# Kernel tuning notes

Hardware: AMD Instinct MI355X
Metric: run time of the kernel (lower is better)

Reference implementation:

```python
import jax, jax.numpy as jnp
import numpy as np

B, P, S, D, H, DFF, VOC = 8, 16, 512, 512, 8, 2048, 10000
DEPTH = D // H
SIGMA = 0.1
T = 256
LN_EPS = 1e-6


def setup_inputs() -> dict:
    key = jax.random.key(0)
    ks = jax.random.split(key, 40)
    n = lambda i, sh, sc=1.0: jax.random.normal(ks[i], sh, jnp.float32) * sc
    inp = {
        "r": n(0, (B, P, D)),
        "x": jax.random.randint(ks[1], (B, 1), 0, VOC),
        "K": n(2, (B, P, S, D)),
        "Vs": n(3, (B, P, S, D)),
        "w": jax.random.uniform(ks[4], (B, P, 1), jnp.float32),
        "I": jax.random.randint(ks[5], (B, P, S), 0, P),
        "t": T,
        "eps_q": n(6, (B, P, 1, D)),
        "eps_k": n(7, (B, P, 1, D)),
        "eps_v": n(8, (B, P, 1, D)),
        "eps_z": n(9, (B, P, 1, D)),
        "gumbel": -jnp.log(-jnp.log(jax.random.uniform(ks[10], (B, P, P), jnp.float32, 1e-8, 1.0))),
        "Wq": n(11, (D, D), 0.02), "bq": jnp.zeros((D,), jnp.float32),
        "Wk": n(12, (D, D), 0.02), "bk": jnp.zeros((D,), jnp.float32),
        "Wv": n(13, (D, D), 0.02), "bv": jnp.zeros((D,), jnp.float32),
        "Wo": n(14, (D, D), 0.02), "bo": jnp.zeros((D,), jnp.float32),
        "ln1_g": jnp.ones((D,), jnp.float32), "ln1_b": jnp.zeros((D,), jnp.float32),
        "ln3_g": jnp.ones((D,), jnp.float32), "ln3_b": jnp.zeros((D,), jnp.float32),
        "W1": n(15, (D, DFF), 0.02), "b1": jnp.zeros((DFF,), jnp.float32),
        "W2": n(16, (DFF, D), 0.02), "b2": jnp.zeros((D,), jnp.float32),
        "Wout": n(17, (D, VOC), 0.02), "bout": jnp.zeros((VOC,), jnp.float32),
    }
    return inp


def _layernorm(x, g, b):
    mu = jnp.mean(x, axis=-1, keepdims=True)
    var = jnp.mean((x - mu) ** 2, axis=-1, keepdims=True)
    return (x - mu) / jnp.sqrt(var + LN_EPS) * g + b


def _split_heads(x):  # (B,P,L,D) -> (B,P,H,L,depth)
    b, p, l, _ = x.shape
    return x.reshape(b, p, l, H, DEPTH).transpose(0, 1, 3, 2, 4)


def _resample(params, i_t, t):  # reorder particle axis on prefix [:t+1]
    pref = jnp.take_along_axis(params[:, :, :t + 1], i_t[:, :, None, None], axis=1)
    return jnp.concatenate([pref, params[:, :, t + 1:]], axis=2)


def reference(r, x, K, Vs, w, I, t, eps_q, eps_k, eps_v, eps_z, gumbel,
              Wq, bq, Wk, bk, Wv, bv, Wo, bo, ln1_g, ln1_b, ln3_g, ln3_b,
              W1, b1, W2, b2, Wout, bout):
    x = x.astype(jnp.int32)
    I = I.astype(jnp.int32)
    r4 = r[:, :, None, :]                                   # (B,P,1,D)
    # --- mha_smc: noisy projections + K/V buffer update at t ---
    q = r4 @ Wq + bq + SIGMA * eps_q
    k = r4 @ Wk + bk + SIGMA * eps_k
    v = r4 @ Wv + bv + SIGMA * eps_v
    K = K.at[:, :, t, :].set(k[:, :, 0, :])
    Vs = Vs.at[:, :, t, :].set(v[:, :, 0, :])
    qh = _split_heads(q)                                    # (B,P,H,1,depth)
    Kh = _split_heads(K)                                    # (B,P,H,S,depth)
    Vh = _split_heads(Vs)
    scores = jnp.einsum('bphqd,bphsd->bphqs', qh, Kh) / jnp.sqrt(jnp.float32(DEPTH))
    mask = (jnp.arange(S) <= t)[None, None, None, None, :]
    scores = jnp.where(mask, scores, jnp.float32(-1e9))
    attn = jax.nn.softmax(scores, axis=-1)                  # (B,P,H,1,S)
    zh = jnp.einsum('bphqs,bphsd->bphqd', attn, Vh)
    z = zh.transpose(0, 1, 3, 2, 4).reshape(B, P, 1, D) @ Wo + bo
    z = z + SIGMA * eps_z                                   # reparametrized output noise
    attn_weights = jnp.mean(attn, axis=2)                   # (B,P,1,S)
    # --- residual + FFN (dropout disabled: training=False) ---
    out1 = _layernorm(z + r4, ln1_g, ln1_b)
    ffn = jnp.maximum(out1 @ W1 + b1, 0.0) @ W2 + b2
    r_ = _layernorm(ffn + out1, ln3_g, ln3_b)
    predictions = r_ @ Wout + bout                          # (B,P,1,VOC)
    # --- classification importance weights ---
    probs = jax.nn.softmax(predictions, axis=-1)
    idx = jnp.broadcast_to(x.reshape(B, 1, 1, 1), (B, P, 1, 1))
    w_sq = jnp.take_along_axis(probs, idx, axis=-1)[:, :, 0, 0]  # (B,P)
    w_sq = jax.lax.stop_gradient(w_sq)
    pred2 = predictions[:, :, 0, :]                         # (B,P,VOC)
    w_for_pred = w_sq[:, :, None]
    good_avg_pred = jnp.mean(pred2, axis=1, keepdims=True)  # (B,1,VOC)
    avg_pred_after_softmax = jnp.mean(jax.nn.softmax(pred2, axis=-1), axis=1, keepdims=True)
    argmax_w = jnp.argmax(w_for_pred, axis=1)               # (B,1)
    max_prediction = jnp.take_along_axis(pred2, argmax_w[:, :, None], axis=1)  # (B,1,VOC)
    # --- sample_and_keep_indices: Gumbel-max categorical over particles ---
    logits = jnp.log(w_sq + 1e-10)                          # (B,P)
    i_t = jnp.argmax(logits[:, None, :] + gumbel, axis=-1).astype(jnp.int32)  # (B,P)
    I_pref = jnp.take_along_axis(I[:, :, :t], i_t[:, :, None], axis=1)
    I_new = jnp.concatenate([I_pref, i_t[:, :, None], I[:, :, t + 1:]], axis=2)
    # --- resampling (faithful to original: V resampled from already-resampled K) ---
    K = _resample(K, i_t, t)
    Vs = _resample(K, i_t, t)
    z = jnp.take_along_axis(z, I_new[:, :, t][:, :, None, None], axis=1)
    w_new = w_sq[:, :, None]
    return (r4, z, avg_pred_after_softmax, good_avg_pred, max_prediction,
            eps_z, attn_weights, K, Vs, w_new, I_new)
```

## Files before the change

### kernel.cpp

```cpp
#include <hip/hip_runtime.h>

#define NDFF 2048
#define NVOC 10000
#define SIGMA 0.1f

typedef float f32x4 __attribute__((ext_vector_type(4)));

#define O0 0
#define O1 65536
#define O2 131072
#define O3 211072
#define O4 291072
#define O5 371072
#define O6 436608
#define O7 502144
#define O8 34056576
#define O9 67611008
#define O10 67611136

#define WQ    0
#define WK    65536
#define WV    131072
#define WZH   196608
#define WZ    262144
#define WO1   327680
#define WH1   393216
#define WPRED 720896
#define WMAX  2000896
#define WSUM  2001024
#define WWSQ  2001152
#define WIT   2001280
#define WF2P  2001536
#define WSC   2263680

__device__ __forceinline__ void copy_sgt(const float* __restrict__ Kin,
                                         float* __restrict__ out, int t,
                                         int q, int bid, int nblk, int tid, int nthr)
{
    const f32x4* K4 = (const f32x4*)Kin;
    f32x4* oK = (f32x4*)(out + O7);
    f32x4* oV = (f32x4*)(out + O8);
    int cnt = 511 - t;
    long totalc = (long)128 * cnt * 128;
    long q0 = (totalc * q) >> 2, q1 = (totalc * (q + 1)) >> 2;
    for (long j = q0 + (long)bid * nthr + tid; j < q1; j += (long)nblk * nthr) {
        int lane = (int)(j & 127);
        long row = j >> 7;
        int bp = (int)(row / cnt);
        int s = t + 1 + (int)(row - (long)bp * cnt);
        long i = ((long)(bp * 512 + s) << 7) + lane;
        f32x4 v = __builtin_nontemporal_load(&K4[i]);
        __builtin_nontemporal_store(v, &oK[i]);
        __builtin_nontemporal_store(v, &oV[i]);
    }
}

__global__ __launch_bounds__(512)
void k_qkv(const float* __restrict__ r,
           const float* __restrict__ Wq, const float* __restrict__ bq, const float* __restrict__ eq, float* __restrict__ oq,
           const float* __restrict__ Wk, const float* __restrict__ bk, const float* __restrict__ ek, float* __restrict__ ok,
           const float* __restrict__ Wv, const float* __restrict__ bv, const float* __restrict__ ev, float* __restrict__ ov)
{
    const float *W, *bias, *eps; float* out;
    if (blockIdx.z == 0)      { W = Wq; bias = bq; eps = eq; out = oq; }
    else if (blockIdx.z == 1) { W = Wk; bias = bk; eps = ek; out = ok; }
    else                      { W = Wv; bias = bv; eps = ev; out = ov; }
    int tid = threadIdx.x;
    int col = tid & 63, kq = tid >> 6;
    int colg = blockIdx.x * 64 + col;
    int row0 = blockIdx.y * 8;
    __shared__ float rs[8][512];
#pragma unroll
    for (int j = 0; j < 8; j++) rs[j][tid & 511] = r[(row0 + j) * 512 + tid];
    __syncthreads();
    float acc[8] = {0,0,0,0,0,0,0,0};
    const float* Wp = W + (kq * 64) * 512 + colg;
#pragma unroll 8
    for (int d = 0; d < 64; d++) {
        float wv = Wp[d * 512];
#pragma unroll
        for (int p = 0; p < 8; p++) acc[p] += rs[p][kq * 64 + d] * wv;
    }
    __syncthreads();
    float (*part)[8][64] = (float(*)[8][64])rs;
#pragma unroll
    for (int p = 0; p < 8; p++) part[kq][p][col] = acc[p];
    __syncthreads();
    {
        int p = tid >> 6, c = tid & 63;
        int cg = blockIdx.x * 64 + c;
        float v = 0.f;
#pragma unroll
        for (int k = 0; k < 8; k++) v += part[k][p][c];
        out[(row0 + p) * 512 + cg] = v + bias[cg] + SIGMA * eps[(row0 + p) * 512 + cg];
    }
}

__global__ __launch_bounds__(512)
void k_attn(const float* __restrict__ qws, const float* __restrict__ kws,
            const float* __restrict__ vws, const float* __restrict__ Kin,
            const float* __restrict__ Vin, const int* __restrict__ t_ptr,
            float* __restrict__ zh, float* __restrict__ scw)
{
    int t = *t_ptr;
    int bp = blockIdx.x, h = blockIdx.y;
    int tid = threadIdx.x;
    int wave = tid >> 6, lane = tid & 63;
    __shared__ float sc[512];
    __shared__ float red[8], red2[8];
    __shared__ float part[8][64];

    float4 qv = ((const float4*)(qws + bp * 512 + h * 64))[lane & 15];

    for (int sb = wave * 4; sb <= t; sb += 32) {
        int s = sb + (lane >> 4);
        bool valid = (s <= t);
        int ss = valid ? s : t;
        const float4* kr = (ss == t) ? (const float4*)(kws + bp * 512 + h * 64)
                                     : (const float4*)(Kin + (bp * 512 + ss) * 512 + h * 64);
        float4 kv = kr[lane & 15];
        float p = qv.x * kv.x + qv.y * kv.y + qv.z * kv.z + qv.w * kv.w;
#pragma unroll
        for (int m = 1; m < 16; m <<= 1) p += __shfl_xor(p, m, 64);
        if ((lane & 15) == 0 && valid) sc[s] = p * 0.125f;
    }
    __syncthreads();

    float lm = -3.0e38f;
    for (int s = tid; s <= t; s += 512) lm = fmaxf(lm, sc[s]);
#pragma unroll
    for (int o = 32; o; o >>= 1) lm = fmaxf(lm, __shfl_xor(lm, o, 64));
    if (lane == 0) red[wave] = lm;
    __syncthreads();
    float m = red[0];
#pragma unroll
    for (int i = 1; i < 8; i++) m = fmaxf(m, red[i]);
    float ls = 0.f;
    for (int s = tid; s <= t; s += 512) ls += __expf(sc[s] - m);
#pragma unroll
    for (int o = 32; o; o >>= 1) ls += __shfl_xor(ls, o, 64);
    if (lane == 0) red2[wave] = ls;
    __syncthreads();
    float tot = 0.f;
#pragma unroll
    for (int i = 0; i < 8; i++) tot += red2[i];
    float inv = 1.f / tot;
    for (int s = tid; s <= t; s += 512) {
        float a = __expf(sc[s] - m) * inv;
        sc[s] = a;
        scw[(bp * 8 + h) * 512 + s] = a;
    }
    __syncthreads();

    float acc = 0.f;
    const float* Vp = Vin + (bp * 512) * 512 + h * 64 + lane;
    int s = wave;
    for (; s + 24 < t; s += 32) {
        float v0 = __builtin_nontemporal_load(Vp + (size_t)(s     ) * 512);
        float v1 = __builtin_nontemporal_load(Vp + (size_t)(s +  8) * 512);
        float v2 = __builtin_nontemporal_load(Vp + (size_t)(s + 16) * 512);
        float v3 = __builtin_nontemporal_load(Vp + (size_t)(s + 24) * 512);
        acc += sc[s] * v0 + sc[s + 8] * v1 + sc[s + 16] * v2 + sc[s + 24] * v3;
    }
    for (; s < t; s += 8) acc += sc[s] * __builtin_nontemporal_load(Vp + (size_t)s * 512);
    if ((t & 7) == wave) acc += sc[t] * vws[bp * 512 + h * 64 + lane];
    part[wave][lane] = acc;
    __syncthreads();
    if (tid < 64) {
        float v = 0.f;
#pragma unroll
        for (int k = 0; k < 8; k++) v += part[k][tid];
        zh[bp * 512 + h * 64 + tid] = v;
    }
}

__global__ __launch_bounds__(512)
void k_zproj(const float* __restrict__ zh, const float* __restrict__ Wo,
             const float* __restrict__ bo, const float* __restrict__ epsz,
             const float* __restrict__ Kin, const int* __restrict__ t_ptr,
             float* __restrict__ outbuf, float* __restrict__ out)
{
    if (blockIdx.x >= 8) {
        int bid = (blockIdx.x - 8) * 16 + blockIdx.y;
        copy_sgt(Kin, outbuf, *t_ptr, 0, bid, 64, threadIdx.x, 512);
        return;
    }
    int tid = threadIdx.x;
    int col = tid & 63, kq = tid >> 6;
    int colg = blockIdx.x * 64 + col;
    int row0 = blockIdx.y * 8;
    __shared__ float rs[8][512];
#pragma unroll
    for (int j = 0; j < 8; j++) rs[j][tid] = zh[(row0 + j) * 512 + tid];
    __syncthreads();
    float acc[8] = {0,0,0,0,0,0,0,0};
    const float* Wp = Wo + (kq * 64) * 512 + colg;
#pragma unroll 8
    for (int d = 0; d < 64; d++) {
        float wv = Wp[d * 512];
#pragma unroll
        for (int p = 0; p < 8; p++) acc[p] += rs[p][kq * 64 + d] * wv;
    }
    __syncthreads();
    float (*part)[8][64] = (float(*)[8][64])rs;
#pragma unroll
    for (int p = 0; p < 8; p++) part[kq][p][col] = acc[p];
    __syncthreads();
    {
        int p = tid >> 6, c = tid & 63;
        int cg = blockIdx.x * 64 + c;
        float v = 0.f;
#pragma unroll
        for (int k = 0; k < 8; k++) v += part[k][p][c];
        out[(row0 + p) * 512 + cg] = v + bo[cg] + SIGMA * epsz[(row0 + p) * 512 + cg];
    }
}

__global__ __launch_bounds__(512)
void k_ffn1(const float* __restrict__ zp, const float* __restrict__ r,
            const float* __restrict__ g, const float* __restrict__ be,
            const float* __restrict__ W1, const float* __restrict__ b1,
            const float* __restrict__ Kin, const int* __restrict__ t_ptr,
            float* __restrict__ outbuf,
            float* __restrict__ o1, float* __restrict__ h1)
{
    if (blockIdx.x >= 32) {
        int bid = (blockIdx.x - 32) * 16 + blockIdx.y;
        copy_sgt(Kin, outbuf, *t_ptr, 1, bid, 64, threadIdx.x, 512);
        return;
    }
    int tid = threadIdx.x;
    int col = tid & 63, kq = tid >> 6;
    int colg = blockIdx.x * 64 + col;
    int row0 = blockIdx.y * 8;
    __shared__ float rs[8][512];
    __shared__ float sm[8], si[8];
    int wave = tid >> 6, lane = tid & 63;
#pragma unroll
    for (int j = 0; j < 8; j++) {
        int gi = (row0 + j) * 512 + tid;
        rs[j][tid] = zp[gi] + r[gi];
    }
    __syncthreads();
    {
        float s = 0.f;
        for (int c = lane; c < 512; c += 64) s += rs[wave][c];
#pragma unroll
        for (int o = 32; o; o >>= 1) s += __shfl_xor(s, o, 64);
        float mu = s * (1.f / 512.f);
        float v = 0.f;
        for (int c = lane; c < 512; c += 64) { float dx = rs[wave][c] - mu; v += dx * dx; }
#pragma unroll
        for (int o = 32; o; o >>= 1) v += __shfl_xor(v, o, 64);
        if (lane == 0) { sm[wave] = mu; si[wave] = rsqrtf(v * (1.f / 512.f) + 1e-6f); }
    }
    __syncthreads();
#pragma unroll
    for (int j = 0; j < 8; j++) {
        float val = (rs[j][tid] - sm[j]) * si[j] * g[tid] + be[tid];
        rs[j][tid] = val;
        if (blockIdx.x == 0) o1[(row0 + j) * 512 + tid] = val;
    }
    __syncthreads();
    float acc[8] = {0,0,0,0,0,0,0,0};
    const float* Wp = W1 + (kq * 64) * NDFF + colg;
#pragma unroll 8
    for (int d = 0; d < 64; d++) {
        float wv = Wp[d * NDFF];
#pragma unroll
        for (int p = 0; p < 8; p++) acc[p] += rs[p][kq * 64 + d] * wv;
    }
    __syncthreads();
    float (*part)[8][64] = (float(*)[8][64])rs;
#pragma unroll
    for (int p = 0; p < 8; p++) part[kq][p][col] = acc[p];
    __syncthreads();
    {
        int p = tid >> 6, c = tid & 63;
        int cg = blockIdx.x * 64 + c;
        float v = 0.f;
#pragma unroll
        for (int k = 0; k < 8; k++) v += part[k][p][c];
        h1[(row0 + p) * NDFF + cg] = fmaxf(v + b1[cg], 0.f);
    }
}

__global__ __launch_bounds__(512)
void k_ffn2p(const float* __restrict__ h1, const float* __restrict__ W2,
             const float* __restrict__ Kin, const int* __restrict__ t_ptr,
             float* __restrict__ outbuf, float* __restrict__ f2p)
{
    if (blockIdx.x >= 8) {
        int bid = blockIdx.y * 4 + blockIdx.z;
        copy_sgt(Kin, outbuf, *t_ptr, 2, bid, 64, threadIdx.x, 512);
        return;
    }
    int tid = threadIdx.x;
    int col = tid & 63, kq = tid >> 6;
    int colg = blockIdx.x * 64 + col;
    int row0 = blockIdx.y * 8;
    int ks = blockIdx.z;
    __shared__ float rs[8][512];
#pragma unroll
    for (int j = 0; j < 8; j++)
        rs[j][tid] = h1[(row0 + j) * NDFF + ks * 512 + tid];
    __syncthreads();
    float acc[8] = {0,0,0,0,0,0,0,0};
    const float* Wp = W2 + (ks * 512 + kq * 64) * 512 + colg;
#pragma unroll 8
    for (int d = 0; d < 64; d++) {
        float wv = Wp[d * 512];
#pragma unroll
        for (int p = 0; p < 8; p++) acc[p] += rs[p][kq * 64 + d] * wv;
    }
    __syncthreads();
    float (*part)[8][64] = (float(*)[8][64])rs;
#pragma unroll
    for (int p = 0; p < 8; p++) part[kq][p][col] = acc[p];
    __syncthreads();
    {
        int p = tid >> 6, c = tid & 63;
        int cg = blockIdx.x * 64 + c;
        float v = 0.f;
#pragma unroll
        for (int k = 0; k < 8; k++) v += part[k][p][c];
        f2p[ks * 65536 + (row0 + p) * 512 + cg] = v;
    }
}

__global__ __launch_bounds__(512)
void k_pred(const float* __restrict__ f2p, const float* __restrict__ b2,
            const float* __restrict__ o1, const float* __restrict__ g3,
            const float* __restrict__ b3, const float* __restrict__ Wout,
            const float* __restrict__ bout,
            const float* __restrict__ Kin, const int* __restrict__ t_ptr,
            float* __restrict__ outbuf, float* __restrict__ pred)
{
    if (blockIdx.x >= 40) {
        int bid = (blockIdx.x - 40) * 8 + blockIdx.y;
        copy_sgt(Kin, outbuf, *t_ptr, 3, bid, 64, threadIdx.x, 512);
        return;
    }
    int tid = threadIdx.x;
    int col = tid & 255, kh = tid >> 8;
    int colg = blockIdx.x * 256 + col;
    int colL = min(colg, NVOC - 1);
    int row0 = blockIdx.y * 16;
    __shared__ float rs[16][512];
    __shared__ float sm[16], si[16];
    int wave = tid >> 6, lane = tid & 63;
#pragma unroll
    for (int j = 0; j < 16; j++) {
        int gi = (row0 + j) * 512 + tid;
        rs[j][tid] = f2p[gi] + f2p[65536 + gi] + f2p[131072 + gi] + f2p[196608 + gi]
                   + b2[tid] + o1[gi];
    }
    __syncthreads();
    {
        int row = wave * 2 + (lane >> 5);
        int l = lane & 31;
        float s = 0.f;
        for (int c = l; c < 512; c += 32) s += rs[row][c];
#pragma unroll
        for (int o = 16; o; o >>= 1) s += __shfl_xor(s, o, 64);
        float mu = s * (1.f / 512.f);
        float v = 0.f;
        for (int c = l; c < 512; c += 32) { float dx = rs[row][c] - mu; v += dx * dx; }
#pragma unroll
        for (int o = 16; o; o >>= 1) v += __shfl_xor(v, o, 64);
        if (l == 0) { sm[row] = mu; si[row] = rsqrtf(v * (1.f / 512.f) + 1e-6f); }
    }
    __syncthreads();
#pragma unroll
    for (int j = 0; j < 16; j++)
        rs[j][tid] = (rs[j][tid] - sm[j]) * si[j] * g3[tid] + b3[tid];
    __syncthreads();
    float acc[16];
#pragma unroll
    for (int p = 0; p < 16; p++) acc[p] = 0.f;
    const float* Wp = Wout + (kh * 256) * NVOC + colL;
#pragma unroll 4
    for (int d = 0; d < 256; d++) {
        float wv = Wp[d * NVOC];
#pragma unroll
        for (int p = 0; p < 16; p++) acc[p] += rs[p][kh * 256 + d] * wv;
    }
    __syncthreads();
    float (*part)[256] = (float(*)[256])rs;
    if (kh == 1) {
#pragma unroll
        for (int p = 0; p < 16; p++) part[p][col] = acc[p];
    }
    __syncthreads();
    if (kh == 0 && colg < NVOC) {
        float bv = bout[colg];
#pragma unroll
        for (int p = 0; p < 16; p++)
            pred[(row0 + p) * NVOC + colg] = acc[p] + part[p][col] + bv;
    }
}

__global__ __launch_bounds__(512)
void k_soft(const float* __restrict__ pred, const int* __restrict__ x,
            const float* __restrict__ scw, const int* __restrict__ t_ptr,
            float* __restrict__ rowmax, float* __restrict__ rowsum,
            float* __restrict__ wsq, float* __restrict__ out)
{
    __shared__ float red[8];
    int row = blockIdx.x, tid = threadIdx.x;
    {
        int t = *t_ptr;
        float a = 0.f;
        if (tid <= t) {
#pragma unroll
            for (int hh = 0; hh < 8; hh++) a += scw[(row * 8 + hh) * 512 + tid];
            a *= 0.125f;
        }
        out[O6 + row * 512 + tid] = a;
    }
    const float* pr = pred + row * NVOC;
    float m = -3.0e38f;
    for (int v = tid; v < NVOC; v += 512) m = fmaxf(m, pr[v]);
#pragma unroll
    for (int o = 32; o; o >>= 1) m = fmaxf(m, __shfl_xor(m, o, 64));
    if ((tid & 63) == 0) red[tid >> 6] = m;
    __syncthreads();
#pragma unroll
    for (int i = 0; i < 8; i++) m = fmaxf(m, red[i]);
    __syncthreads();
    float s = 0.f;
    for (int v = tid; v < NVOC; v += 512) s += __expf(pr[v] - m);
#pragma unroll
    for (int o = 32; o; o >>= 1) s += __shfl_xor(s, o, 64);
    if ((tid & 63) == 0) red[tid >> 6] = s;
    __syncthreads();
    if (tid == 0) {
        float tot = 0.f;
#pragma unroll
        for (int i = 0; i < 8; i++) tot += red[i];
        rowmax[row] = m; rowsum[row] = tot;
        int b = row >> 4;
        float w = __expf(pr[x[b]] - m) / tot;
        wsq[row] = w;
        out[O9 + row] = w;
    }
}

__global__ __launch_bounds__(512)
void k_vocab(const float* __restrict__ pred, const float* __restrict__ rowmax,
             const float* __restrict__ rowsum, const float* __restrict__ wsq,
             const float* __restrict__ gumbel, int* __restrict__ it,
             float* __restrict__ out)
{
    int b = blockIdx.y;
    int tid = threadIdx.x;
    __shared__ int s_amw;
    if (tid == 0) {
        float bw = -3.0e38f; int bj = 0;
#pragma unroll
        for (int pp = 0; pp < 16; pp++) {
            float wv = wsq[b * 16 + pp];
            if (wv > bw) { bw = wv; bj = pp; }
        }
        s_amw = bj;
    }
    if (blockIdx.x == 0 && tid < 16) {
        float best = -3.0e38f; int bi = 0;
#pragma unroll
        for (int pp = 0; pp < 16; pp++) {
            float v = logf(wsq[b * 16 + pp] + 1e-10f) + gumbel[(b * 16 + tid) * 16 + pp];
            if (v > best) { best = v; bi = pp; }
        }
        it[b * 16 + tid] = bi;
    }
    __syncthreads();
    int v = blockIdx.x * 512 + tid;
    if (v >= NVOC) return;
    int amw = s_amw;
    float ga = 0.f, as = 0.f;
#pragma unroll
    for (int p = 0; p < 16; p++) {
        int rr = b * 16 + p;
        float pv = pred[rr * NVOC + v];
        ga += pv;
        as += __expf(pv - rowmax[rr]) * (1.f / rowsum[rr]);
    }
    out[O3 + b * NVOC + v] = ga * (1.f / 16.f);
    out[O2 + b * NVOC + v] = as * (1.f / 16.f);
    out[O4 + b * NVOC + v] = pred[(b * 16 + amw) * NVOC + v];
}

__global__ __launch_bounds__(256)
void k_resample(const float* __restrict__ Kin, const float* __restrict__ kws,
                const int* __restrict__ it, const int* __restrict__ t_ptr,
                const float* __restrict__ r, const float* __restrict__ epsz,
                const float* __restrict__ zws, const int* __restrict__ Iin,
                float* __restrict__ out)
{
    int t = *t_ptr;
    const f32x4* K4  = (const f32x4*)Kin;
    const f32x4* kw4 = (const f32x4*)kws;
    const f32x4* r4  = (const f32x4*)r;
    const f32x4* e4  = (const f32x4*)epsz;
    const f32x4* z4  = (const f32x4*)zws;
    f32x4* oK = (f32x4*)(out + O7);
    f32x4* oV = (f32x4*)(out + O8);
    int cnt = t + 1;
    long total = (long)128 * cnt * 128;
    long total2 = total + 16384;
    for (long j = (long)blockIdx.x * 256 + threadIdx.x; j < total2; j += (long)gridDim.x * 256) {
        if (j < total) {
            int lane = (int)(j & 127);
            long row = j >> 7;
            int bp = (int)(row / cnt);
            int s = (int)(row - (long)bp * cnt);
            int b = bp >> 4;
            int ip = it[bp];
            int ip2 = it[b * 16 + ip];
            f32x4 vK, vV;
            if (s == t) {
                vK = kw4[(b * 16 + ip) * 128 + lane];
                vV = kw4[(b * 16 + ip2) * 128 + lane];
            } else {
                vK = K4[((long)((b * 16 + ip) * 512 + s) << 7) + lane];
                vV = K4[((long)((b * 16 + ip2) * 512 + s) << 7) + lane];
            }
            long i = ((long)(bp * 512 + s) << 7) + lane;
            __builtin_nontemporal_store(vK, &oK[i]);
            __builtin_nontemporal_store(vV, &oV[i]);
        } else {
            int jj = (int)(j - total);
            int fidx = jj * 4;
            ((f32x4*)(out + O0))[jj] = r4[jj];
            ((f32x4*)(out + O5))[jj] = e4[jj];
            int row = fidx >> 9, d0 = fidx & 511;
            int b = row >> 4;
            int ip = it[row];
            ((f32x4*)(out + O1))[jj] = z4[((b * 16 + ip) << 7) + (d0 >> 2)];
#pragma unroll
            for (int k = 0; k < 4; k++) {
                int s = d0 + k;
                float iv;
                if (s < t)       iv = (float)Iin[((b * 16 + ip) << 9) + s];
                else if (s == t) iv = (float)ip;
                else             iv = (float)Iin[row * 512 + s];
                out[O10 + fidx + k] = iv;
            }
        }
    }
}

extern "C" void kernel_launch(void* const* d_in, const int* in_sizes, int n_in,
                              void* d_out, int out_size, void* d_ws, size_t ws_size,
                              hipStream_t stream) {
    const float* r      = (const float*)d_in[0];
    const int*   x      = (const int*)d_in[1];
    const float* Kin    = (const float*)d_in[2];
    const float* Vin    = (const float*)d_in[3];
    const int*   Iin    = (const int*)d_in[5];
    const int*   t_ptr  = (const int*)d_in[6];
    const float* eps_q  = (const float*)d_in[7];
    const float* eps_k  = (const float*)d_in[8];
    const float* eps_v  = (const float*)d_in[9];
    const float* eps_z  = (const float*)d_in[10];
    const float* gumbel = (const float*)d_in[11];
    const float* Wq = (const float*)d_in[12]; const float* bq = (const float*)d_in[13];
    const float* Wk = (const float*)d_in[14]; const float* bk = (const float*)d_in[15];
    const float* Wv = (const float*)d_in[16]; const float* bv = (const float*)d_in[17];
    const float* Wo = (const float*)d_in[18]; const float* bo = (const float*)d_in[19];
    const float* ln1_g = (const float*)d_in[20]; const float* ln1_b = (const float*)d_in[21];
    const float* ln3_g = (const float*)d_in[22]; const float* ln3_b = (const float*)d_in[23];
    const float* W1 = (const float*)d_in[24]; const float* b1 = (const float*)d_in[25];
    const float* W2 = (const float*)d_in[26]; const float* b2 = (const float*)d_in[27];
    const float* Wout = (const float*)d_in[28]; const float* bout = (const float*)d_in[29];

    float* ws  = (float*)d_ws;
    float* q   = ws + WQ;
    float* kv  = ws + WK;
    float* vv  = ws + WV;
    float* zh  = ws + WZH;
    float* zp  = ws + WZ;
    float* o1  = ws + WO1;
    float* h1  = ws + WH1;
    float* pr  = ws + WPRED;
    float* rmx = ws + WMAX;
    float* rsm = ws + WSUM;
    float* wsq = ws + WWSQ;
    int*   itw = (int*)(ws + WIT);
    float* f2p = ws + WF2P;
    float* scw = ws + WSC;
    float* outp = (float*)d_out;

    k_qkv<<<dim3(8, 16, 3), 512, 0, stream>>>(r, Wq, bq, eps_q, q, Wk, bk, eps_k, kv, Wv, bv, eps_v, vv);
    k_attn<<<dim3(128, 8), 512, 0, stream>>>(q, kv, vv, Kin, Vin, t_ptr, zh, scw);
    k_zproj<<<dim3(12, 16), 512, 0, stream>>>(zh, Wo, bo, eps_z, Kin, t_ptr, outp, zp);
    k_ffn1<<<dim3(36, 16), 512, 0, stream>>>(zp, r, ln1_g, ln1_b, W1, b1, Kin, t_ptr, outp, o1, h1);
    k_ffn2p<<<dim3(9, 16, 4), 512, 0, stream>>>(h1, W2, Kin, t_ptr, outp, f2p);
    k_pred<<<dim3(48, 8), 512, 0, stream>>>(f2p, b2, o1, ln3_g, ln3_b, Wout, bout, Kin, t_ptr, outp, pr);
    k_soft<<<128, 512, 0, stream>>>(pr, x, scw, t_ptr, rmx, rsm, wsq, outp);
    k_vocab<<<dim3(20, 8), 512, 0, stream>>>(pr, rmx, rsm, wsq, gumbel, itw, outp);
    k_resample<<<2048, 256, 0, stream>>>(Kin, kv, itw, t_ptr, r, eps_z, zp, Iin, outp);
}
```

Measured before the change: 232.6 us.

## Move K/V tail copy entirely into the attention kernel's extra blocks

The bulk copy of K rows beyond t into both K and V outputs was spread in quarters across the zproj, ffn1, ffn2p and pred kernels. It now runs entirely in 256 extra blocks appended to the attention launch, and the other kernels shrink to their compute grids. The aim is to overlap the bandwidth-bound copy with the attention kernel, which is itself memory-heavy, and keep the small GEMM kernels lean. The risk is that the copy competes with attention for HBM bandwidth and lengthens that kernel, where before it was hidden behind several latency-bound GEMM kernels.

```diff
diff --git a/kernel.cpp b/kernel.cpp
--- a/kernel.cpp
+++ b/kernel.cpp
@@ -33,28 +33,6 @@
 #define WF2P  2001536
 #define WSC   2263680
 
-__device__ __forceinline__ void copy_sgt(const float* __restrict__ Kin,
-                                         float* __restrict__ out, int t,
-                                         int q, int bid, int nblk, int tid, int nthr)
-{
-    const f32x4* K4 = (const f32x4*)Kin;
-    f32x4* oK = (f32x4*)(out + O7);
-    f32x4* oV = (f32x4*)(out + O8);
-    int cnt = 511 - t;
-    long totalc = (long)128 * cnt * 128;
-    long q0 = (totalc * q) >> 2, q1 = (totalc * (q + 1)) >> 2;
-    for (long j = q0 + (long)bid * nthr + tid; j < q1; j += (long)nblk * nthr) {
-        int lane = (int)(j & 127);
-        long row = j >> 7;
-        int bp = (int)(row / cnt);
-        int s = t + 1 + (int)(row - (long)bp * cnt);
-        long i = ((long)(bp * 512 + s) << 7) + lane;
-        f32x4 v = __builtin_nontemporal_load(&K4[i]);
-        __builtin_nontemporal_store(v, &oK[i]);
-        __builtin_nontemporal_store(v, &oV[i]);
-    }
-}
-
 __global__ __launch_bounds__(512)
 void k_qkv(const float* __restrict__ r,
            const float* __restrict__ Wq, const float* __restrict__ bq, const float* __restrict__ eq, float* __restrict__ oq,
@@ -100,9 +78,30 @@
 void k_attn(const float* __restrict__ qws, const float* __restrict__ kws,
             const float* __restrict__ vws, const float* __restrict__ Kin,
             const float* __restrict__ Vin, const int* __restrict__ t_ptr,
-            float* __restrict__ zh, float* __restrict__ scw)
+            float* __restrict__ zh, float* __restrict__ scw,
+            float* __restrict__ outfull)
 {
     int t = *t_ptr;
+    if (blockIdx.x >= 128) {
+        int bid = (blockIdx.x - 128) * 8 + blockIdx.y;
+        int tid = threadIdx.x;
+        const f32x4* K4 = (const f32x4*)Kin;
+        f32x4* oK = (f32x4*)(outfull + O7);
+        f32x4* oV = (f32x4*)(outfull + O8);
+        int cnt = 511 - t;
+        long totalc = (long)128 * cnt * 128;
+        for (long j = (long)bid * 512 + tid; j < totalc; j += (long)256 * 512) {
+            int lane = (int)(j & 127);
+            long row = j >> 7;
+            int bp = (int)(row / cnt);
+            int s = t + 1 + (int)(row - (long)bp * cnt);
+            long i = ((long)(bp * 512 + s) << 7) + lane;
+            f32x4 v = __builtin_nontemporal_load(&K4[i]);
+            __builtin_nontemporal_store(v, &oK[i]);
+            __builtin_nontemporal_store(v, &oV[i]);
+        }
+        return;
+    }
     int bp = blockIdx.x, h = blockIdx.y;
     int tid = threadIdx.x;
     int wave = tid >> 6, lane = tid & 63;
@@ -177,14 +176,8 @@
 __global__ __launch_bounds__(512)
 void k_zproj(const float* __restrict__ zh, const float* __restrict__ Wo,
              const float* __restrict__ bo, const float* __restrict__ epsz,
-             const float* __restrict__ Kin, const int* __restrict__ t_ptr,
-             float* __restrict__ outbuf, float* __restrict__ out)
-{
-    if (blockIdx.x >= 8) {
-        int bid = (blockIdx.x - 8) * 16 + blockIdx.y;
-        copy_sgt(Kin, outbuf, *t_ptr, 0, bid, 64, threadIdx.x, 512);
-        return;
-    }
+             float* __restrict__ out)
+{
     int tid = threadIdx.x;
     int col = tid & 63, kq = tid >> 6;
     int colg = blockIdx.x * 64 + col;
@@ -220,15 +213,8 @@
 void k_ffn1(const float* __restrict__ zp, const float* __restrict__ r,
             const float* __restrict__ g, const float* __restrict__ be,
             const float* __restrict__ W1, const float* __restrict__ b1,
-            const float* __restrict__ Kin, const int* __restrict__ t_ptr,
-            float* __restrict__ outbuf,
             float* __restrict__ o1, float* __restrict__ h1)
 {
-    if (blockIdx.x >= 32) {
-        int bid = (blockIdx.x - 32) * 16 + blockIdx.y;
-        copy_sgt(Kin, outbuf, *t_ptr, 1, bid, 64, threadIdx.x, 512);
-        return;
-    }
     int tid = threadIdx.x;
     int col = tid & 63, kq = tid >> 6;
     int colg = blockIdx.x * 64 + col;
@@ -287,14 +273,8 @@
 
 __global__ __launch_bounds__(512)
 void k_ffn2p(const float* __restrict__ h1, const float* __restrict__ W2,
-             const float* __restrict__ Kin, const int* __restrict__ t_ptr,
-             float* __restrict__ outbuf, float* __restrict__ f2p)
-{
-    if (blockIdx.x >= 8) {
-        int bid = blockIdx.y * 4 + blockIdx.z;
-        copy_sgt(Kin, outbuf, *t_ptr, 2, bid, 64, threadIdx.x, 512);
-        return;
-    }
+             float* __restrict__ f2p)
+{
     int tid = threadIdx.x;
     int col = tid & 63, kq = tid >> 6;
     int colg = blockIdx.x * 64 + col;
@@ -332,15 +312,8 @@
 void k_pred(const float* __restrict__ f2p, const float* __restrict__ b2,
             const float* __restrict__ o1, const float* __restrict__ g3,
             const float* __restrict__ b3, const float* __restrict__ Wout,
-            const float* __restrict__ bout,
-            const float* __restrict__ Kin, const int* __restrict__ t_ptr,
-            float* __restrict__ outbuf, float* __restrict__ pred)
-{
-    if (blockIdx.x >= 40) {
-        int bid = (blockIdx.x - 40) * 8 + blockIdx.y;
-        copy_sgt(Kin, outbuf, *t_ptr, 3, bid, 64, threadIdx.x, 512);
-        return;
-    }
+            const float* __restrict__ bout, float* __restrict__ pred)
+{
     int tid = threadIdx.x;
     int col = tid & 255, kh = tid >> 8;
     int colg = blockIdx.x * 256 + col;
@@ -592,11 +565,11 @@
     float* outp = (float*)d_out;
 
     k_qkv<<<dim3(8, 16, 3), 512, 0, stream>>>(r, Wq, bq, eps_q, q, Wk, bk, eps_k, kv, Wv, bv, eps_v, vv);
-    k_attn<<<dim3(128, 8), 512, 0, stream>>>(q, kv, vv, Kin, Vin, t_ptr, zh, scw);
-    k_zproj<<<dim3(12, 16), 512, 0, stream>>>(zh, Wo, bo, eps_z, Kin, t_ptr, outp, zp);
-    k_ffn1<<<dim3(36, 16), 512, 0, stream>>>(zp, r, ln1_g, ln1_b, W1, b1, Kin, t_ptr, outp, o1, h1);
-    k_ffn2p<<<dim3(9, 16, 4), 512, 0, stream>>>(h1, W2, Kin, t_ptr, outp, f2p);
-    k_pred<<<dim3(48, 8), 512, 0, stream>>>(f2p, b2, o1, ln3_g, ln3_b, Wout, bout, Kin, t_ptr, outp, pr);
+    k_attn<<<dim3(160, 8), 512, 0, stream>>>(q, kv, vv, Kin, Vin, t_ptr, zh, scw, outp);
+    k_zproj<<<dim3(8, 16), 512, 0, stream>>>(zh, Wo, bo, eps_z, zp);
+    k_ffn1<<<dim3(32, 16), 512, 0, stream>>>(zp, r, ln1_g, ln1_b, W1, b1, o1, h1);
+    k_ffn2p<<<dim3(8, 16, 4), 512, 0, stream>>>(h1, W2, f2p);
+    k_pred<<<dim3(40, 8), 512, 0, stream>>>(f2p, b2, o1, ln3_g, ln3_b, Wout, bout, pr);
     k_soft<<<128, 512, 0, stream>>>(pr, x, scw, t_ptr, rmx, rsm, wsq, outp);
     k_vocab<<<dim3(20, 8), 512, 0, stream>>>(pr, rmx, rsm, wsq, gumbel, itw, outp);
     k_resample<<<2048, 256, 0, stream>>>(Kin, kv, itw, t_ptr, r, eps_z, zp, Iin, outp);
```

Result: faster. 218.4 us (-6.1%).
